# Performance work log

Hardware: AMD Instinct MI355X
Metric: run time of the kernel (lower is better)

## Reference

```python
import jax, jax.numpy as jnp
import numpy as np

N, D, E, C = 8192, 64, 524288, 2


def setup_inputs() -> dict:
    key = jax.random.key(0)
    ks = jax.random.split(key, 14)
    src = jax.random.randint(ks[0], (E,), 0, N, dtype=jnp.int32)
    dst = jax.random.randint(ks[1], (E,), 0, N, dtype=jnp.int32)
    h = jax.random.normal(ks[2], (N, D), jnp.float32)
    # dense adjacency consistent with the edge list (A[u,v]=1 for edge u->v)
    one = jnp.ones((E,), jnp.float32)
    A = jnp.zeros((N, N), jnp.float32).at[src, dst].max(one)
    # motif adjacencies: random subsets of the base edges
    keep1 = jax.random.bernoulli(ks[3], 0.5, (E,)).astype(jnp.float32)
    keep2 = jax.random.bernoulli(ks[4], 0.3, (E,)).astype(jnp.float32)
    A1 = jnp.zeros((N, N), jnp.float32).at[src, dst].max(keep1)
    A2 = jnp.zeros((N, N), jnp.float32).at[src, dst].max(keep2)
    s = 0.05
    Ww = jax.random.normal(ks[5], (D, D), jnp.float32) * s
    Wb = jax.random.normal(ks[6], (D,), jnp.float32) * s
    fc0 = jax.random.normal(ks[7], (D, D), jnp.float32) * s
    fc1 = jax.random.normal(ks[8], (D, D), jnp.float32) * s
    fc2 = jax.random.normal(ks[9], (D, D), jnp.float32) * s
    lin_w = jax.random.normal(ks[10], (3 * D, C), jnp.float32) * s
    lin_b = jax.random.normal(ks[11], (C,), jnp.float32) * s
    return {"h": h, "A": A, "A1": A1, "A2": A2, "Ww": Ww, "Wb": Wb,
            "fc0": fc0, "fc1": fc1, "fc2": fc2, "lin_w": lin_w,
            "lin_b": lin_b, "src": src, "dst": dst}


def _dot_gat_pool(az, fc, src, dst, emask, nmask):
    # DGL DotGatConv (num_heads=1): ft = fc(az); e_uv = <ft_u, ft_v>/sqrt(F);
    # edge-softmax per destination; sum-aggregate; then avg-pool over subgraph nodes.
    n = az.shape[0]
    ft = az @ fc                                   # [N, F]
    scale = 1.0 / jnp.sqrt(jnp.float32(ft.shape[-1]))
    e = jnp.sum(ft[src] * ft[dst], axis=-1) * scale  # [E]
    neg = jnp.finfo(e.dtype).min
    e = jnp.where(emask, e, neg)
    m = jax.ops.segment_max(e, dst, num_segments=n)
    m = jnp.where(jnp.isfinite(m), m, 0.0)
    ex = jnp.where(emask, jnp.exp(e - m[dst]), 0.0)
    den = jax.ops.segment_sum(ex, dst, num_segments=n)
    alpha = ex / jnp.maximum(den[dst], 1e-9)       # [E]
    agg = jax.ops.segment_sum(alpha[:, None] * ft[src], dst, num_segments=n)  # [N, F]
    # mean over nodes present in the (motif) subgraph
    return jnp.sum(agg * nmask[:, None], axis=0) / jnp.maximum(jnp.sum(nmask), 1.0)


def reference(h, A, A1, A2, Ww, Wb, fc0, fc1, fc2, lin_w, lin_b, src, dst):
    n = h.shape[0]
    Z = (A @ h) @ Ww.T + Wb                        # Z = W(A h)
    outs = []
    # motif 0: full edge set, az = Z
    all_e = jnp.ones(src.shape, bool)
    all_n = jnp.ones((n,), jnp.float32)
    outs.append(_dot_gat_pool(Z, fc0, src, dst, all_e, all_n))
    # motifs 1, 2: edge subgraph where A_k[u, v] > 0, az = A_k @ Z
    for Ak, fck in ((A1, fc1), (A2, fc2)):
        emask = Ak[src, dst] > 0
        em = emask.astype(jnp.float32)
        nmask = jnp.zeros((n,), jnp.float32).at[src].max(em)
        nmask = jnp.maximum(nmask, jnp.zeros((n,), jnp.float32).at[dst].max(em))
        az = Ak @ Z
        outs.append(_dot_gat_pool(az, fck, src, dst, emask, nmask))
    feat = jnp.concatenate(outs)[None, :]          # [1, 3*F]
    return feat @ lin_w + lin_b                    # [1, num_classes]
```

## Files before the change

### kernel.cpp

```cpp
#include <hip/hip_runtime.h>

constexpr int N = 8192;
constexpr int D = 64;
constexpr int E = 524288;
constexpr int ND = N * D;
constexpr int CAP = 192;

constexpr size_t SZ_BITMAP = (size_t)N * (size_t)N / 8;
constexpr size_t SZ_CNT    = (size_t)N * sizeof(int);
constexpr size_t O_BITMAP  = 0;
constexpr size_t O_SRCCNT  = O_BITMAP + SZ_BITMAP;
constexpr size_t O_DSTCNT  = O_SRCCNT + SZ_CNT;
constexpr size_t O_NF1     = O_DSTCNT + SZ_CNT;
constexpr size_t O_NF2     = O_NF1 + N;
constexpr size_t O_POOLED  = O_NF2 + N;
constexpr size_t O_BETA    = O_POOLED + 1024;
constexpr size_t ZERO_END  = O_BETA + 3 * (size_t)N * 4;
constexpr size_t O_BKTS    = ZERO_END;
constexpr size_t O_BKTD    = O_BKTS + (size_t)N * CAP * 4;
constexpr size_t O_Z       = O_BKTD + (size_t)N * CAP * 4;
constexpr size_t O_FT      = O_Z + (size_t)N * D * 4;


__global__ void __launch_bounds__(256) edge_classify_fill(
        const int* __restrict__ src, const int* __restrict__ dst,
        const float* __restrict__ A1, const float* __restrict__ A2,
        unsigned* __restrict__ bitmap,
        int* __restrict__ srcCnt, int* __restrict__ dstCnt,
        unsigned char* __restrict__ nf1, unsigned char* __restrict__ nf2,
        int* __restrict__ bktS, int* __restrict__ bktD) {
    int i = blockIdx.x * blockDim.x + threadIdx.x;
    if (i >= E) return;
    int u = src[i], v = dst[i];
    long long key = ((long long)u << 13) | v;
    unsigned bit = 1u << (key & 31);
    unsigned old = atomicOr(&bitmap[key >> 5], bit);
    int own = ((old & bit) == 0) ? 1 : 0;
    float a1 = A1[key];
    float a2 = A2[key];
    int f1 = (a1 > 0.0f) ? 1 : 0;
    int f2 = (a2 > 0.0f) ? 1 : 0;
    int f12 = f1 | (f2 << 1);
    if (own) {
        int p = atomicAdd(&srcCnt[u], 1);
        if (p < CAP) bktS[u * CAP + p] = v | (f12 << 13);
    }
    int p2 = atomicAdd(&dstCnt[v], 1);
    if (p2 < CAP) bktD[v * CAP + p2] = u | (f12 << 13);
    if (f1) { nf1[u] = 1; nf1[v] = 1; }
    if (f2) { nf2[u] = 1; nf2[v] = 1; }
}

__global__ void __launch_bounds__(256) rowpipe1(
        const int* __restrict__ srcCnt, const int* __restrict__ bktS,
        const float* __restrict__ h, const float* __restrict__ Ww,
        const float* __restrict__ Wb, const float* __restrict__ fc0,
        float* __restrict__ Z, float* __restrict__ ft0) {
    __shared__ float W1[64 * 64];
    __shared__ float W2[64 * 64];
    int t = threadIdx.x;
    for (int i = t; i < 4096; i += 256) {
        int r = i >> 6, c = i & 63;
        W1[i] = Ww[c * 64 + r];
        W2[i] = fc0[i];
    }
    __syncthreads();
    int wid = t >> 6, lane = t & 63;
    int row = blockIdx.x * 4 + wid;
    int b = row * CAP, e = b + min(srcCnt[row], CAP);
    float a0 = 0.0f, a1 = 0.0f, a2 = 0.0f, a3 = 0.0f;
    int j = b;
    for (; j + 3 < e; j += 4) {
        int u0 = bktS[j] & 8191, u1 = bktS[j + 1] & 8191;
        int u2 = bktS[j + 2] & 8191, u3 = bktS[j + 3] & 8191;
        a0 += h[(size_t)u0 * D + lane];
        a1 += h[(size_t)u1 * D + lane];
        a2 += h[(size_t)u2 * D + lane];
        a3 += h[(size_t)u3 * D + lane];
    }
    for (; j < e; ++j) a0 += h[(size_t)(bktS[j] & 8191) * D + lane];
    float ah = (a0 + a1) + (a2 + a3);
    float z = Wb[lane];
    #pragma unroll 8
    for (int k = 0; k < 64; ++k)
        z = fmaf(__shfl(ah, k), W1[k * 64 + lane], z);
    Z[(size_t)row * D + lane] = z;
    float f = 0.0f;
    #pragma unroll 8
    for (int k = 0; k < 64; ++k)
        f = fmaf(__shfl(z, k), W2[k * 64 + lane], f);
    ft0[(size_t)row * D + lane] = f;
}

__global__ void __launch_bounds__(256) rowpipe2(
        const int* __restrict__ srcCnt, const int* __restrict__ bktS,
        const float* __restrict__ Z,
        const float* __restrict__ fc1, const float* __restrict__ fc2,
        float* __restrict__ ft1, float* __restrict__ ft2) {
    __shared__ float W1[64 * 64];
    __shared__ float W2[64 * 64];
    int t = threadIdx.x;
    for (int i = t; i < 4096; i += 256) {
        W1[i] = fc1[i];
        W2[i] = fc2[i];
    }
    __syncthreads();
    int wid = t >> 6, lane = t & 63;
    int row = blockIdx.x * 4 + wid;
    int b = row * CAP, e = b + min(srcCnt[row], CAP);
    float a1x = 0.0f, a2x = 0.0f, a1y = 0.0f, a2y = 0.0f;
    int j = b;
    for (; j + 1 < e; j += 2) {
        int e0 = bktS[j], e1 = bktS[j + 1];
        if (e0 >> 13) {
            float z = Z[(size_t)(e0 & 8191) * D + lane];
            if (e0 & (1 << 13)) a1x += z;
            if (e0 & (1 << 14)) a2x += z;
        }
        if (e1 >> 13) {
            float z = Z[(size_t)(e1 & 8191) * D + lane];
            if (e1 & (1 << 13)) a1y += z;
            if (e1 & (1 << 14)) a2y += z;
        }
    }
    for (; j < e; ++j) {
        int e0 = bktS[j];
        if (e0 >> 13) {
            float z = Z[(size_t)(e0 & 8191) * D + lane];
            if (e0 & (1 << 13)) a1x += z;
            if (e0 & (1 << 14)) a2x += z;
        }
    }
    float s1 = a1x + a1y, s2 = a2x + a2y;
    float f1 = 0.0f, f2 = 0.0f;
    #pragma unroll 8
    for (int k = 0; k < 64; ++k) {
        f1 = fmaf(__shfl(s1, k), W1[k * 64 + lane], f1);
        f2 = fmaf(__shfl(s2, k), W2[k * 64 + lane], f2);
    }
    ft1[(size_t)row * D + lane] = f1;
    ft2[(size_t)row * D + lane] = f2;
}

__device__ __forceinline__ void sddmm3(
        const float* __restrict__ ft0,
        const float4* __restrict__ fq0, const float4* __restrict__ fq1,
        const float4* __restrict__ fq2,
        int ent, bool valid, float& s0, float& s1, float& s2) {
    s0 = -3.0e38f; s1 = -3.0e38f; s2 = -3.0e38f;
    if (!valid) return;
    int u = ent & 8191;
    const float4* pu = (const float4*)(ft0 + (size_t)u * D);
    {
        float d0 = 0.0f, d1 = 0.0f;
        #pragma unroll
        for (int k = 0; k < 16; k += 2) {
            float4 a = pu[k], bq = fq0[k];
            float4 c = pu[k + 1], dq = fq0[k + 1];
            d0 = fmaf(a.x, bq.x, d0); d0 = fmaf(a.y, bq.y, d0);
            d0 = fmaf(a.z, bq.z, d0); d0 = fmaf(a.w, bq.w, d0);
            d1 = fmaf(c.x, dq.x, d1); d1 = fmaf(c.y, dq.y, d1);
            d1 = fmaf(c.z, dq.z, d1); d1 = fmaf(c.w, dq.w, d1);
        }
        s0 = (d0 + d1) * 0.125f;
    }
    if (ent & (1 << 13)) {
        const float4* p1 = pu + ND / 4;
        float d0 = 0.0f, d1 = 0.0f;
        #pragma unroll
        for (int k = 0; k < 16; k += 2) {
            float4 a = p1[k], bq = fq1[k];
            float4 c = p1[k + 1], dq = fq1[k + 1];
            d0 = fmaf(a.x, bq.x, d0); d0 = fmaf(a.y, bq.y, d0);
            d0 = fmaf(a.z, bq.z, d0); d0 = fmaf(a.w, bq.w, d0);
            d1 = fmaf(c.x, dq.x, d1); d1 = fmaf(c.y, dq.y, d1);
            d1 = fmaf(c.z, dq.z, d1); d1 = fmaf(c.w, dq.w, d1);
        }
        s1 = (d0 + d1) * 0.125f;
    }
    if (ent & (1 << 14)) {
        const float4* p2 = pu + 2 * (ND / 4);
        float d0 = 0.0f, d1 = 0.0f;
        #pragma unroll
        for (int k = 0; k < 16; k += 2) {
            float4 a = p2[k], bq = fq2[k];
            float4 c = p2[k + 1], dq = fq2[k + 1];
            d0 = fmaf(a.x, bq.x, d0); d0 = fmaf(a.y, bq.y, d0);
            d0 = fmaf(a.z, bq.z, d0); d0 = fmaf(a.w, bq.w, d0);
            d1 = fmaf(c.x, dq.x, d1); d1 = fmaf(c.y, dq.y, d1);
            d1 = fmaf(c.z, dq.z, d1); d1 = fmaf(c.w, dq.w, d1);
        }
        s2 = (d0 + d1) * 0.125f;
    }
}

__global__ void __launch_bounds__(256) gat_alpha(
        const float* __restrict__ ftAll, const int* __restrict__ dstCnt,
        const int* __restrict__ bktD, float* __restrict__ beta) {
    int t = threadIdx.x, wid = t >> 6, lane = t & 63;
    int row = blockIdx.x * 4 + wid;
    __shared__ float fv[4][3][64];
    const float* ft0 = ftAll;
    fv[wid][0][lane] = ft0[(size_t)row * D + lane];
    fv[wid][1][lane] = ft0[ND + (size_t)row * D + lane];
    fv[wid][2][lane] = ft0[2 * ND + (size_t)row * D + lane];
    const float4* fq0 = (const float4*)fv[wid][0];
    const float4* fq1 = (const float4*)fv[wid][1];
    const float4* fq2 = (const float4*)fv[wid][2];
    int b = row * CAP, e = b + min(dstCnt[row], CAP);
    int nch = (e - b + 63) >> 6;
    float w0r[4], w1r[4], w2r[4];
    int entr[4];
    float mr0 = -3.0e38f, mr1 = -3.0e38f, mr2 = -3.0e38f;
    for (int c = 0; c < nch; ++c) {
        int j = b + c * 64 + lane;
        bool valid = j < e;
        int ent = valid ? (bktD[j] | (1 << 15)) : 0;
        float s0, s1, s2;
        sddmm3(ft0, fq0, fq1, fq2, ent, valid, s0, s1, s2);
        if (c < 4) { w0r[c] = s0; w1r[c] = s1; w2r[c] = s2; entr[c] = ent; }
        float c0 = s0, c1 = s1, c2 = s2;
        c0 = fmaxf(c0, __shfl_xor(c0, 1));  c1 = fmaxf(c1, __shfl_xor(c1, 1));  c2 = fmaxf(c2, __shfl_xor(c2, 1));
        c0 = fmaxf(c0, __shfl_xor(c0, 2));  c1 = fmaxf(c1, __shfl_xor(c1, 2));  c2 = fmaxf(c2, __shfl_xor(c2, 2));
        c0 = fmaxf(c0, __shfl_xor(c0, 4));  c1 = fmaxf(c1, __shfl_xor(c1, 4));  c2 = fmaxf(c2, __shfl_xor(c2, 4));
        c0 = fmaxf(c0, __shfl_xor(c0, 8));  c1 = fmaxf(c1, __shfl_xor(c1, 8));  c2 = fmaxf(c2, __shfl_xor(c2, 8));
        c0 = fmaxf(c0, __shfl_xor(c0, 16)); c1 = fmaxf(c1, __shfl_xor(c1, 16)); c2 = fmaxf(c2, __shfl_xor(c2, 16));
        c0 = fmaxf(c0, __shfl_xor(c0, 32)); c1 = fmaxf(c1, __shfl_xor(c1, 32)); c2 = fmaxf(c2, __shfl_xor(c2, 32));
        mr0 = fmaxf(mr0, c0); mr1 = fmaxf(mr1, c1); mr2 = fmaxf(mr2, c2);
    }
    float den0 = 0.0f, den1 = 0.0f, den2 = 0.0f;
    for (int c = 0; c < nch; ++c) {
        float s0, s1, s2; int ent;
        if (c < 4) { s0 = w0r[c]; s1 = w1r[c]; s2 = w2r[c]; ent = entr[c]; }
        else {
            int j = b + c * 64 + lane;
            bool valid = j < e;
            ent = valid ? (bktD[j] | (1 << 15)) : 0;
            sddmm3(ft0, fq0, fq1, fq2, ent, valid, s0, s1, s2);
        }
        float w0 = (ent & (1 << 15)) ? __expf(s0 - mr0) : 0.0f;
        float w1 = (ent & (1 << 13)) ? __expf(s1 - mr1) : 0.0f;
        float w2 = (ent & (1 << 14)) ? __expf(s2 - mr2) : 0.0f;
        if (c < 4) { w0r[c] = w0; w1r[c] = w1; w2r[c] = w2; }
        float t0 = w0, t1 = w1, t2 = w2;
        t0 += __shfl_xor(t0, 1);  t1 += __shfl_xor(t1, 1);  t2 += __shfl_xor(t2, 1);
        t0 += __shfl_xor(t0, 2);  t1 += __shfl_xor(t1, 2);  t2 += __shfl_xor(t2, 2);
        t0 += __shfl_xor(t0, 4);  t1 += __shfl_xor(t1, 4);  t2 += __shfl_xor(t2, 4);
        t0 += __shfl_xor(t0, 8);  t1 += __shfl_xor(t1, 8);  t2 += __shfl_xor(t2, 8);
        t0 += __shfl_xor(t0, 16); t1 += __shfl_xor(t1, 16); t2 += __shfl_xor(t2, 16);
        t0 += __shfl_xor(t0, 32); t1 += __shfl_xor(t1, 32); t2 += __shfl_xor(t2, 32);
        den0 += t0; den1 += t1; den2 += t2;
    }
    float i0 = 1.0f / fmaxf(den0, 1e-9f);
    float i1 = 1.0f / fmaxf(den1, 1e-9f);
    float i2 = 1.0f / fmaxf(den2, 1e-9f);
    for (int c = 0; c < nch; ++c) {
        float w0, w1, w2; int ent;
        if (c < 4) { w0 = w0r[c]; w1 = w1r[c]; w2 = w2r[c]; ent = entr[c]; }
        else {
            int j = b + c * 64 + lane;
            bool valid = j < e;
            ent = valid ? (bktD[j] | (1 << 15)) : 0;
            float s0, s1, s2;
            sddmm3(ft0, fq0, fq1, fq2, ent, valid, s0, s1, s2);
            w0 = (ent & (1 << 15)) ? __expf(s0 - mr0) : 0.0f;
            w1 = (ent & (1 << 13)) ? __expf(s1 - mr1) : 0.0f;
            w2 = (ent & (1 << 14)) ? __expf(s2 - mr2) : 0.0f;
        }
        int u = ent & 8191;
        if (w0 > 0.0f) atomicAdd(&beta[u], w0 * i0);
        if (w1 > 0.0f) atomicAdd(&beta[N + u], w1 * i1);
        if (w2 > 0.0f) atomicAdd(&beta[2 * N + u], w2 * i2);
    }
}

__global__ void __launch_bounds__(256) pool_dense(
        const float* __restrict__ ftAll, const float* __restrict__ beta,
        float* __restrict__ pooled) {
    int t = threadIdx.x, wid = t >> 6, lane = t & 63;
    float a0 = 0.0f, a1 = 0.0f, a2 = 0.0f;
    for (int u = blockIdx.x * 4 + wid; u < N; u += gridDim.x * 4) {
        float b0 = beta[u], b1 = beta[N + u], b2 = beta[2 * N + u];
        const float* p = ftAll + (size_t)u * D + lane;
        a0 = fmaf(b0, p[0], a0);
        a1 = fmaf(b1, p[ND], a1);
        a2 = fmaf(b2, p[2 * ND], a2);
    }
    __shared__ float red[3][256];
    red[0][t] = a0; red[1][t] = a1; red[2][t] = a2;
    __syncthreads();
    if (wid < 3) {
        float s = red[wid][lane] + red[wid][64 + lane] + red[wid][128 + lane] + red[wid][192 + lane];
        atomicAdd(&pooled[wid * 64 + lane], s);
    }
}

__global__ void __launch_bounds__(256) final_kernel(
        const float* __restrict__ pooled,
        const unsigned char* __restrict__ nf1, const unsigned char* __restrict__ nf2,
        const float* __restrict__ lin_w, const float* __restrict__ lin_b,
        float* __restrict__ out) {
    __shared__ int r1[256], r2[256];
    __shared__ float feat[192];
    __shared__ int cnt[2];
    int t = threadIdx.x;
    int s1 = 0, s2 = 0;
    for (int i = t; i < N; i += 256) { s1 += nf1[i]; s2 += nf2[i]; }
    r1[t] = s1; r2[t] = s2;
    __syncthreads();
    for (int off = 128; off > 0; off >>= 1) {
        if (t < off) { r1[t] += r1[t + off]; r2[t] += r2[t + off]; }
        __syncthreads();
    }
    if (t == 0) { cnt[0] = r1[0]; cnt[1] = r2[0]; }
    __syncthreads();
    if (t < 192) {
        int sel = t >> 6;
        float div = (sel == 0) ? (float)N : fmaxf((float)cnt[sel - 1], 1.0f);
        feat[t] = pooled[t] / div;
    }
    __syncthreads();
    if (t < 2) {
        float o = lin_b[t];
        for (int k = 0; k < 192; ++k) o = fmaf(feat[k], lin_w[k * 2 + t], o);
        out[t] = o;
    }
}

extern "C" void kernel_launch(void* const* d_in, const int* in_sizes, int n_in,
                              void* d_out, int out_size, void* d_ws, size_t ws_size,
                              hipStream_t stream) {
    const float* h   = (const float*)d_in[0];
    const float* A1  = (const float*)d_in[2];
    const float* A2  = (const float*)d_in[3];
    const float* Ww  = (const float*)d_in[4];
    const float* Wb  = (const float*)d_in[5];
    const float* fc0 = (const float*)d_in[6];
    const float* fc1 = (const float*)d_in[7];
    const float* fc2 = (const float*)d_in[8];
    const float* lw  = (const float*)d_in[9];
    const float* lb  = (const float*)d_in[10];
    const int* src   = (const int*)d_in[11];
    const int* dst   = (const int*)d_in[12];
    float* out = (float*)d_out;

    char* w = (char*)d_ws;
    unsigned* bitmap   = (unsigned*)(w + O_BITMAP);
    int* srcCnt        = (int*)(w + O_SRCCNT);
    int* dstCnt        = (int*)(w + O_DSTCNT);
    unsigned char* nf1 = (unsigned char*)(w + O_NF1);
    unsigned char* nf2 = (unsigned char*)(w + O_NF2);
    float* pooled      = (float*)(w + O_POOLED);
    float* beta        = (float*)(w + O_BETA);
    int* bktS          = (int*)(w + O_BKTS);
    int* bktD          = (int*)(w + O_BKTD);
    float* Z           = (float*)(w + O_Z);
    float* ftAll       = (float*)(w + O_FT);
    float* ft1         = ftAll + (size_t)ND;
    float* ft2         = ftAll + 2 * (size_t)ND;

    hipMemsetAsync(w, 0, ZERO_END, stream);

    edge_classify_fill<<<E / 256, 256, 0, stream>>>(src, dst, A1, A2, bitmap,
                                                    srcCnt, dstCnt, nf1, nf2, bktS, bktD);

    rowpipe1<<<N / 4, 256, 0, stream>>>(srcCnt, bktS, h, Ww, Wb, fc0, Z, ftAll);
    rowpipe2<<<N / 4, 256, 0, stream>>>(srcCnt, bktS, Z, fc1, fc2, ft1, ft2);

    gat_alpha<<<N / 4, 256, 0, stream>>>(ftAll, dstCnt, bktD, beta);
    pool_dense<<<256, 256, 0, stream>>>(ftAll, beta, pooled);

    final_kernel<<<1, 256, 0, stream>>>(pooled, nf1, nf2, lw, lb, out);
}
```

Before: 753.3 us.

## Replace global bitmap dedup with per-row shared-memory duplicate marking

Drops the N×N bitmap and its per-edge atomicOr, so the memset no longer clears that large region. Source buckets now receive every edge, and rowpipe1 finds duplicate neighbours per row with a quadratic scan in shared memory. It then marks them with a DUP bit that rowpipe1 and rowpipe2 skip. This adds per-row scan work and takes bucket capacity from duplicate entries.

```diff
diff --git a/kernel.cpp b/kernel.cpp
--- a/kernel.cpp
+++ b/kernel.cpp
@@ -5,11 +5,10 @@
 constexpr int E = 524288;
 constexpr int ND = N * D;
 constexpr int CAP = 192;
-
-constexpr size_t SZ_BITMAP = (size_t)N * (size_t)N / 8;
+constexpr int DUP = 1 << 16;
+
 constexpr size_t SZ_CNT    = (size_t)N * sizeof(int);
-constexpr size_t O_BITMAP  = 0;
-constexpr size_t O_SRCCNT  = O_BITMAP + SZ_BITMAP;
+constexpr size_t O_SRCCNT  = 0;
 constexpr size_t O_DSTCNT  = O_SRCCNT + SZ_CNT;
 constexpr size_t O_NF1     = O_DSTCNT + SZ_CNT;
 constexpr size_t O_NF2     = O_NF1 + N;
@@ -22,10 +21,9 @@
 constexpr size_t O_FT      = O_Z + (size_t)N * D * 4;
 
 
-__global__ void __launch_bounds__(256) edge_classify_fill(
+__global__ void __launch_bounds__(256) edge_fill(
         const int* __restrict__ src, const int* __restrict__ dst,
         const float* __restrict__ A1, const float* __restrict__ A2,
-        unsigned* __restrict__ bitmap,
         int* __restrict__ srcCnt, int* __restrict__ dstCnt,
         unsigned char* __restrict__ nf1, unsigned char* __restrict__ nf2,
         int* __restrict__ bktS, int* __restrict__ bktD) {
@@ -33,18 +31,13 @@
     if (i >= E) return;
     int u = src[i], v = dst[i];
     long long key = ((long long)u << 13) | v;
-    unsigned bit = 1u << (key & 31);
-    unsigned old = atomicOr(&bitmap[key >> 5], bit);
-    int own = ((old & bit) == 0) ? 1 : 0;
     float a1 = A1[key];
     float a2 = A2[key];
     int f1 = (a1 > 0.0f) ? 1 : 0;
     int f2 = (a2 > 0.0f) ? 1 : 0;
     int f12 = f1 | (f2 << 1);
-    if (own) {
-        int p = atomicAdd(&srcCnt[u], 1);
-        if (p < CAP) bktS[u * CAP + p] = v | (f12 << 13);
-    }
+    int p = atomicAdd(&srcCnt[u], 1);
+    if (p < CAP) bktS[u * CAP + p] = v | (f12 << 13);
     int p2 = atomicAdd(&dstCnt[v], 1);
     if (p2 < CAP) bktD[v * CAP + p2] = u | (f12 << 13);
     if (f1) { nf1[u] = 1; nf1[v] = 1; }
@@ -52,33 +45,49 @@
 }
 
 __global__ void __launch_bounds__(256) rowpipe1(
-        const int* __restrict__ srcCnt, const int* __restrict__ bktS,
+        const int* __restrict__ srcCnt, int* __restrict__ bktS,
         const float* __restrict__ h, const float* __restrict__ Ww,
         const float* __restrict__ Wb, const float* __restrict__ fc0,
         float* __restrict__ Z, float* __restrict__ ft0) {
     __shared__ float W1[64 * 64];
     __shared__ float W2[64 * 64];
+    __shared__ int vb[4][CAP];
     int t = threadIdx.x;
     for (int i = t; i < 4096; i += 256) {
         int r = i >> 6, c = i & 63;
         W1[i] = Ww[c * 64 + r];
         W2[i] = fc0[i];
     }
-    __syncthreads();
     int wid = t >> 6, lane = t & 63;
     int row = blockIdx.x * 4 + wid;
-    int b = row * CAP, e = b + min(srcCnt[row], CAP);
+    int cnt = min(srcCnt[row], CAP);
+    for (int i = lane; i < cnt; i += 64) vb[wid][i] = bktS[row * CAP + i];
+    __syncthreads();
+    for (int i = lane; i < cnt; i += 64) {
+        int vi = vb[wid][i] & 8191;
+        bool dup = false;
+        for (int j = 0; j < i; ++j) dup |= ((vb[wid][j] & 8191) == vi);
+        if (dup) {
+            int m = vb[wid][i] | DUP;
+            vb[wid][i] = m;
+            bktS[row * CAP + i] = m;
+        }
+    }
+    __syncthreads();
     float a0 = 0.0f, a1 = 0.0f, a2 = 0.0f, a3 = 0.0f;
-    int j = b;
-    for (; j + 3 < e; j += 4) {
-        int u0 = bktS[j] & 8191, u1 = bktS[j + 1] & 8191;
-        int u2 = bktS[j + 2] & 8191, u3 = bktS[j + 3] & 8191;
-        a0 += h[(size_t)u0 * D + lane];
-        a1 += h[(size_t)u1 * D + lane];
-        a2 += h[(size_t)u2 * D + lane];
-        a3 += h[(size_t)u3 * D + lane];
-    }
-    for (; j < e; ++j) a0 += h[(size_t)(bktS[j] & 8191) * D + lane];
+    int j = 0;
+    for (; j + 3 < cnt; j += 4) {
+        int e0 = vb[wid][j], e1 = vb[wid][j + 1];
+        int e2 = vb[wid][j + 2], e3 = vb[wid][j + 3];
+        if (!(e0 & DUP)) a0 += h[(size_t)(e0 & 8191) * D + lane];
+        if (!(e1 & DUP)) a1 += h[(size_t)(e1 & 8191) * D + lane];
+        if (!(e2 & DUP)) a2 += h[(size_t)(e2 & 8191) * D + lane];
+        if (!(e3 & DUP)) a3 += h[(size_t)(e3 & 8191) * D + lane];
+    }
+    for (; j < cnt; ++j) {
+        int e0 = vb[wid][j];
+        if (!(e0 & DUP)) a0 += h[(size_t)(e0 & 8191) * D + lane];
+    }
     float ah = (a0 + a1) + (a2 + a3);
     float z = Wb[lane];
     #pragma unroll 8
@@ -112,12 +121,12 @@
     int j = b;
     for (; j + 1 < e; j += 2) {
         int e0 = bktS[j], e1 = bktS[j + 1];
-        if (e0 >> 13) {
+        if (((e0 >> 13) & 3) && !(e0 & DUP)) {
             float z = Z[(size_t)(e0 & 8191) * D + lane];
             if (e0 & (1 << 13)) a1x += z;
             if (e0 & (1 << 14)) a2x += z;
         }
-        if (e1 >> 13) {
+        if (((e1 >> 13) & 3) && !(e1 & DUP)) {
             float z = Z[(size_t)(e1 & 8191) * D + lane];
             if (e1 & (1 << 13)) a1y += z;
             if (e1 & (1 << 14)) a2y += z;
@@ -125,7 +134,7 @@
     }
     for (; j < e; ++j) {
         int e0 = bktS[j];
-        if (e0 >> 13) {
+        if (((e0 >> 13) & 3) && !(e0 & DUP)) {
             float z = Z[(size_t)(e0 & 8191) * D + lane];
             if (e0 & (1 << 13)) a1x += z;
             if (e0 & (1 << 14)) a2x += z;
@@ -345,7 +354,6 @@
     float* out = (float*)d_out;
 
     char* w = (char*)d_ws;
-    unsigned* bitmap   = (unsigned*)(w + O_BITMAP);
     int* srcCnt        = (int*)(w + O_SRCCNT);
     int* dstCnt        = (int*)(w + O_DSTCNT);
     unsigned char* nf1 = (unsigned char*)(w + O_NF1);
@@ -361,8 +369,8 @@
 
     hipMemsetAsync(w, 0, ZERO_END, stream);
 
-    edge_classify_fill<<<E / 256, 256, 0, stream>>>(src, dst, A1, A2, bitmap,
-                                                    srcCnt, dstCnt, nf1, nf2, bktS, bktD);
+    edge_fill<<<E / 256, 256, 0, stream>>>(src, dst, A1, A2,
+                                           srcCnt, dstCnt, nf1, nf2, bktS, bktD);
 
     rowpipe1<<<N / 4, 256, 0, stream>>>(srcCnt, bktS, h, Ww, Wb, fc0, Z, ftAll);
     rowpipe2<<<N / 4, 256, 0, stream>>>(srcCnt, bktS, Z, fc1, fc2, ft1, ft2);
```

Measured after the change: 763.5 us. About the same (+1.4%).
